# Performance work log

Measured on AMD Instinct MI355X. Metric: run time of the kernel, lower is better.

The kernel has to match this reference:

```python
import jax, jax.numpy as jnp
import numpy as np

NUM_RBF = 16
MIN_MU = 2.0
MAX_MU = 22.0
K_NEIGHBORS = 48
MAX_REL = 32
POS_DIM = 16
EDGE_OUT = 128
N_TOKENS = 21
N_ATOMS = 14
N_ATOM_TYPES = 5  # N, CA, C, O + 1 virtual
W_NORMAL, W_B1, W_B2 = 0.58273431, -0.56802827, -0.54067466


def setup_inputs() -> dict:
    key = jax.random.key(0)
    ks = jax.random.split(key, 8)
    B, L = 2, 2048
    X = jax.random.normal(ks[0], (B, L, N_ATOMS, 3), jnp.float32) * 10.0
    X_m = jnp.ones((B, L, N_ATOMS), jnp.float32)
    S = jax.random.randint(ks[1], (B, L), 0, N_TOKENS)
    residue_idx = jnp.arange(B * L).reshape(B, L)
    mask = jnp.ones((B, L), jnp.float32)
    # token -> atom-slot index table for [N, CA, C, O] (per-token fancy indexing)
    table = jax.random.randint(ks[2], (N_TOKENS, 4), 0, N_ATOMS)
    n_pos_in = 2 * MAX_REL + 1
    W_pos = jax.random.normal(ks[3], (n_pos_in, POS_DIM), jnp.float32) * 0.05
    b_pos = jnp.zeros((POS_DIM,), jnp.float32)
    n_edge_in = POS_DIM + NUM_RBF * N_ATOM_TYPES * N_ATOM_TYPES  # 416
    W_e = jax.random.normal(ks[4], (n_edge_in, EDGE_OUT), jnp.float32) * 0.05
    ln_g = jnp.ones((EDGE_OUT,), jnp.float32)
    ln_b = jnp.zeros((EDGE_OUT,), jnp.float32)
    return {"X": X, "X_m": X_m, "S": S, "residue_idx": residue_idx, "mask": mask,
            "table": table, "W_pos": W_pos, "b_pos": b_pos, "W_e": W_e,
            "ln_g": ln_g, "ln_b": ln_b}


def _rbf(D):
    mu = jnp.linspace(MIN_MU, MAX_MU, NUM_RBF, dtype=D.dtype)
    sigma = (MAX_MU - MIN_MU) / NUM_RBF
    return jnp.exp(-jnp.square((D[..., None] - mu) / sigma))


def reference(X, X_m, S, residue_idx, mask, table, W_pos, b_pos, W_e, ln_g, ln_b):
    B, L = S.shape
    # token-dependent gather of backbone atoms [B,L,4,3]
    idx = table[S]
    X_bb = jnp.take_along_axis(X, idx[..., None], axis=2)
    N_, CA, C_ = X_bb[:, :, 0], X_bb[:, :, 1], X_bb[:, :, 2]
    # virtual atom (CB-like) from N, CA, C
    b1 = N_ - CA
    b2 = C_ - CA
    nrm = jnp.cross(b1, b2)
    Xv = W_NORMAL * nrm + W_B1 * b1 + W_B2 * b2 + CA
    X_all = jnp.concatenate([X_bb, Xv[:, :, None, :]], axis=2)  # [B,L,5,3]
    # pairwise CA distances + masked top-k neighbors
    diff = CA[:, :, None, :] - CA[:, None, :, :]
    D = jnp.sqrt(jnp.sum(diff * diff, -1) + 1e-6)
    m2 = mask[:, :, None] * mask[:, None, :]
    D_adj = D * m2 + (1.0 - m2) * 1e6
    _, E_idx = jax.lax.top_k(-D_adj, K_NEIGHBORS)  # [B,L,K]
    # gather neighbor atom coords [B,L,K,5,3]
    X_nb = jax.vmap(lambda xa, ei: xa[ei])(X_all, E_idx)
    d = X_all[:, :, None, :, None, :] - X_nb[:, :, :, None, :, :]  # [B,L,K,5,5,3]
    Dab = jnp.sqrt(jnp.sum(d * d, -1) + 1e-6)
    RBF = _rbf(Dab).reshape(B, L, K_NEIGHBORS, N_ATOM_TYPES * N_ATOM_TYPES * NUM_RBF)
    # positional encodings of relative residue offsets
    r_nb = jax.vmap(lambda r, ei: r[ei])(residue_idx, E_idx)
    off = jnp.clip(residue_idx[:, :, None] - r_nb + MAX_REL, 0, 2 * MAX_REL)
    pos = jax.nn.one_hot(off, 2 * MAX_REL + 1, dtype=RBF.dtype) @ W_pos + b_pos
    # edge embedding (no bias) + layernorm
    E = jnp.concatenate([pos, RBF], -1) @ W_e
    mu_ = jnp.mean(E, -1, keepdims=True)
    var = jnp.var(E, -1, keepdims=True)
    E = (E - mu_) * jax.lax.rsqrt(var + 1e-5) * ln_g + ln_b
    return E, E_idx
```

## Files before the change

### kernel.cpp

```cpp
#include <hip/hip_runtime.h>
#include <hip/hip_bf16.h>

#define Bq 2
#define Lq 2048
#define BLq (Bq*Lq)
#define KNB 48
#define NA 14
#define NTOK 21
#define NRBF 16
#define POSD 16
#define EOUT 128
#define CSTRIDE 168
#define ESTRIDE 132
#define E_ELEMS (BLq*KNB*EOUT)

typedef __attribute__((ext_vector_type(8))) short short8;
typedef __attribute__((ext_vector_type(4))) float f32x4;

__device__ __forceinline__ unsigned short bf16_rn(float x) {
    unsigned int u = __float_as_uint(x);
    unsigned int r = (u + 0x7fffu + ((u >> 16) & 1u)) >> 16;
    return (unsigned short)r;
}

__device__ __forceinline__ unsigned int pkbf2(float a, float b) {
    __hip_bfloat162 t = __float22bfloat162_rn(make_float2(a, b));
    union { __hip_bfloat162 h; unsigned int u; } cv; cv.h = t;
    return cv.u;
}

__global__ void prep_kernel(const float* __restrict__ X, const int* __restrict__ S,
                            const int* __restrict__ table, const float* __restrict__ mask,
                            const float* __restrict__ We,
                            float* __restrict__ Xall, float4* __restrict__ CA4,
                            short* __restrict__ Wp) {
    int bid = blockIdx.x;
    if (bid < 16) {
        int t = bid * 256 + threadIdx.x;
        if (t >= BLq) return;
        int s = S[t];
        float bb[4][3];
#pragma unroll
        for (int a = 0; a < 4; ++a) {
            int ia = table[s * 4 + a];
#pragma unroll
            for (int d = 0; d < 3; ++d) bb[a][d] = X[(t * NA + ia) * 3 + d];
        }
        float b1[3], b2[3], nr[3];
#pragma unroll
        for (int d = 0; d < 3; ++d) { b1[d] = bb[0][d] - bb[1][d]; b2[d] = bb[2][d] - bb[1][d]; }
        nr[0] = b1[1] * b2[2] - b1[2] * b2[1];
        nr[1] = b1[2] * b2[0] - b1[0] * b2[2];
        nr[2] = b1[0] * b2[1] - b1[1] * b2[0];
#pragma unroll
        for (int a = 0; a < 4; ++a)
#pragma unroll
            for (int d = 0; d < 3; ++d) Xall[t * 15 + a * 3 + d] = bb[a][d];
#pragma unroll
        for (int d = 0; d < 3; ++d) {
            float xv = 0.58273431f * nr[d] + (-0.56802827f) * b1[d] + (-0.54067466f) * b2[d] + bb[1][d];
            Xall[t * 15 + 12 + d] = xv;
        }
        CA4[t] = make_float4(bb[1][0], bb[1][1], bb[1][2], mask[t]);
    } else {
        int t = (bid - 16) * 256 + threadIdx.x;
        if (t >= 13 * 8 * 64 * 8) return;
        int j = t & 7;
        int lane = (t >> 3) & 63;
        int nt = (t >> 9) & 7;
        int kt = t >> 12;
        int k = kt * 32 + (lane >> 4) * 8 + j;
        int n = nt * 16 + (lane & 15);
        Wp[t] = (short)bf16_rn(We[k * 128 + n]);
    }
}

__device__ __forceinline__ void rbf16(float D, unsigned short* dst) {
    const float s1   = 0.96089793f;
    const float dlt  = 1.28119724f;
    const float dlt2 = 1.64146638f;
    const float tdl  = 2.56239448f;
    const float Cg   = 0.10273972f;
    float u0 = __builtin_fmaf(D, s1, -1.92179585f);
    uint4 qa, qb;
    {
        float ua = u0 - 5.12478895f;
        float va = __builtin_amdgcn_exp2f(-(ua * ua));
        float eu = fminf(__builtin_fmaf(tdl, ua, -dlt2), 120.0f);
        float ed = fminf(__builtin_fmaf(-tdl, ua, -dlt2), 120.0f);
        float gu = __builtin_amdgcn_exp2f(eu);
        float gd = __builtin_amdgcn_exp2f(ed);
        float v4 = va;
        float v5 = v4 * gu; float g2 = gu * Cg;
        float v6 = v5 * g2;
        float v7 = v6 * (g2 * Cg);
        float v3 = v4 * gd; float h2 = gd * Cg;
        float v2 = v3 * h2; float h3 = h2 * Cg;
        float v1 = v2 * h3;
        float v0 = v1 * (h3 * Cg);
        qa.x = pkbf2(v0, v1); qa.y = pkbf2(v2, v3);
        qa.z = pkbf2(v4, v5); qa.w = pkbf2(v6, v7);
    }
    {
        float ub = u0 - 15.37436684f;
        float vb = __builtin_amdgcn_exp2f(-(ub * ub));
        float eu = fminf(__builtin_fmaf(tdl, ub, -dlt2), 120.0f);
        float ed = fminf(__builtin_fmaf(-tdl, ub, -dlt2), 120.0f);
        float gu = __builtin_amdgcn_exp2f(eu);
        float gd = __builtin_amdgcn_exp2f(ed);
        float v12 = vb;
        float v13 = v12 * gu; float g2 = gu * Cg;
        float v14 = v13 * g2;
        float v15 = v14 * (g2 * Cg);
        float v11 = v12 * gd; float h2 = gd * Cg;
        float v10 = v11 * h2; float h3 = h2 * Cg;
        float v9  = v10 * h3;
        float v8  = v9 * (h3 * Cg);
        qb.x = pkbf2(v8, v9);   qb.y = pkbf2(v10, v11);
        qb.z = pkbf2(v12, v13); qb.w = pkbf2(v14, v15);
    }
    *(uint4*)dst = qa;
    *(uint4*)(dst + 8) = qb;
}

__global__ __launch_bounds__(256, 6) void edge_kernel(
    const float4* __restrict__ CA4, const float* __restrict__ Xall,
    const int* __restrict__ ridx, const float* __restrict__ Wpos,
    const float* __restrict__ bpos, const short* __restrict__ Wp,
    const float* __restrict__ lng, const float* __restrict__ lnb,
    float* __restrict__ out, float* __restrict__ out_idx) {
    __shared__ __align__(16) char smem[25344];
    unsigned int* histR = (unsigned int*)smem;
    unsigned int* hist8 = (unsigned int*)smem;
    unsigned long long* buf = (unsigned long long*)(smem + 16384);
    float* Dsm = (float*)smem;
    unsigned short* Asm = (unsigned short*)(smem + 4800);
    float* Xq = (float*)(smem + 20928);
    float* Xn = (float*)(smem + 20992);
    int* offs = (int*)(smem + 23872);
    int* eidxl = (int*)(smem + 24064);
    float* Esm = (float*)smem;
    __shared__ unsigned int nacc, wtot[4];
    __shared__ int sh_bin, sh_excl, sh_cnt;

    int bl = blockIdx.x;
    int base = (bl >> 11) << 11;
    int tid = threadIdx.x;
    int w = tid >> 6, lane = tid & 63;

    float4 q = CA4[bl];
    unsigned long long key[8];
#pragma unroll
    for (int i = 0; i < 8; ++i) {
        int j = tid + (i << 8);
        float4 c = CA4[base + j];
        float dx = __fsub_rn(q.x, c.x);
        float dy = __fsub_rn(q.y, c.y);
        float dz = __fsub_rn(q.z, c.z);
        float s = __fadd_rn(__fadd_rn(__fmul_rn(dx, dx), __fmul_rn(dy, dy)), __fmul_rn(dz, dz));
        float D = __fsqrt_rn(__fadd_rn(s, 1e-6f));
        float m2 = __fmul_rn(q.w, c.w);
        float Dadj = __fadd_rn(__fmul_rn(D, m2), __fmul_rn(__fsub_rn(1.0f, m2), 1000000.0f));
        key[i] = (((unsigned long long)__float_as_uint(Dadj)) << 16) | (unsigned int)j;
    }

    {
        uint4 z = make_uint4(0u, 0u, 0u, 0u);
        for (int i = tid; i < 1024; i += 256) ((uint4*)histR)[i] = z;
    }
    __syncthreads();
#pragma unroll
    for (int i = 0; i < 8; ++i)
        atomicAdd(&histR[(((unsigned int)(key[i] >> 38)) << 2) | (unsigned int)(lane & 3)], 1u);
    __syncthreads();

    unsigned int loc[4], lsum = 0;
#pragma unroll
    for (int j = 0; j < 4; ++j) {
        uint4 r4 = ((const uint4*)histR)[tid * 4 + j];
        loc[j] = r4.x + r4.y + r4.z + r4.w;
        lsum += loc[j];
    }
    unsigned int incl = lsum;
#pragma unroll
    for (int o = 1; o < 64; o <<= 1) {
        unsigned int v = __shfl_up(incl, o);
        if (lane >= o) incl += v;
    }
    if (lane == 63) wtot[w] = incl;
    __syncthreads();
    unsigned int cum = incl - lsum;
#pragma unroll
    for (int u = 0; u < 4; ++u) cum += (u < w) ? wtot[u] : 0u;
#pragma unroll
    for (int j = 0; j < 4; ++j) {
        if ((int)cum < 48 && 48 <= (int)(cum + loc[j])) {
            sh_bin = tid * 4 + j;
            sh_excl = (int)cum;
            sh_cnt = (int)loc[j];
        }
        cum += loc[j];
    }
    __syncthreads();

    unsigned long long prefix = (unsigned long long)(unsigned int)sh_bin;
    int need = 48 - sh_excl;
    int cnt = sh_cnt;
    int shift = 38;

    while (cnt > 80 && shift > 0) {
        shift = (shift >= 8) ? (shift - 8) : 0;
        hist8[tid] = 0;
        __syncthreads();
#pragma unroll
        for (int i = 0; i < 8; ++i)
            if ((key[i] >> (shift + 8)) == prefix)
                atomicAdd(&hist8[(unsigned int)((key[i] >> shift) & 255ull)], 1u);
        __syncthreads();
        if (tid < 64) {
            unsigned int h0 = hist8[4 * tid + 0], h1 = hist8[4 * tid + 1];
            unsigned int h2 = hist8[4 * tid + 2], h3 = hist8[4 * tid + 3];
            unsigned int s4 = h0 + h1 + h2 + h3;
            unsigned int incl2 = s4;
#pragma unroll
            for (int o = 1; o < 64; o <<= 1) {
                unsigned int v = __shfl_up(incl2, o);
                if (tid >= o) incl2 += v;
            }
            unsigned int excl2 = incl2 - s4;
            if ((int)excl2 < need && need <= (int)incl2) {
                unsigned int cb = excl2;
                unsigned int hh[4] = {h0, h1, h2, h3};
                int bsel = 3;
#pragma unroll
                for (int bb2 = 0; bb2 < 4; ++bb2) {
                    if ((int)(cb + hh[bb2]) >= need) { bsel = bb2; break; }
                    cb += hh[bb2];
                }
                sh_bin = 4 * tid + bsel;
                sh_excl = (int)cb;
                sh_cnt = (int)hh[bsel];
            }
        }
        __syncthreads();
        prefix = (prefix << 8) | (unsigned long long)(unsigned int)sh_bin;
        need -= sh_excl;
        cnt = sh_cnt;
    }

    if (tid == 0) nacc = 0;
    __syncthreads();
#pragma unroll
    for (int i = 0; i < 8; ++i) {
        bool p = (key[i] >> shift) <= prefix;
        unsigned long long m = __ballot(p);
        if (m != 0ull) {
            int leader = __ffsll((long long)m) - 1;
            unsigned int bp2 = 0;
            if (lane == leader) bp2 = atomicAdd(&nacc, (unsigned int)__popcll(m));
            bp2 = (unsigned int)__shfl((int)bp2, leader);
            if (p) {
                unsigned int pos = bp2 + (unsigned int)__popcll(m & ((1ull << lane) - 1ull));
                if (pos < 128) buf[pos] = key[i];
            }
        }
    }
    __syncthreads();
    unsigned int mcnt = nacc;
    if (mcnt > 128) mcnt = 128;
    if (tid < 128 && tid >= (int)mcnt) buf[tid] = ~0ULL;
    __syncthreads();

    int mp = (int)((mcnt + 7u) & ~7u);
    if (mp > 128) mp = 128;
    if (tid < 128) {
        unsigned long long k = buf[tid];
        int rank = 0;
        for (int u = 0; u < mp; ++u) rank += (buf[u] < k) ? 1 : 0;
        if (rank < KNB) {
            int j = (int)(k & 0xffffull);
            eidxl[rank] = j;
            out_idx[bl * KNB + rank] = (float)j;
        }
    }
    __syncthreads();

    if (tid < KNB) {
        int j = eidxl[tid];
        int off = ridx[bl] - ridx[base + j] + 32;
        offs[tid] = min(max(off, 0), 64);
    }
    if (tid < 15) Xq[tid] = Xall[bl * 15 + tid];
    for (int f = tid; f < KNB * 15; f += 256) {
        int k = f / 15, d = f - k * 15;
        int j = eidxl[k];
        Xn[f] = Xall[(base + j) * 15 + d];
    }
    __syncthreads();

    for (int f = tid; f < KNB * 25; f += 256) {
        int k = f / 25, p = f - k * 25;
        int a = p / 5, c = p - a * 5;
        float dx = Xq[a * 3 + 0] - Xn[k * 15 + c * 3 + 0];
        float dy = Xq[a * 3 + 1] - Xn[k * 15 + c * 3 + 1];
        float dz = Xq[a * 3 + 2] - Xn[k * 15 + c * 3 + 2];
        Dsm[f] = sqrtf(dx * dx + dy * dy + dz * dz + 1e-6f);
    }
    __syncthreads();

    int quad = lane >> 4, lr = lane & 15;
    f32x4 acc[3][2];
#pragma unroll
    for (int mt = 0; mt < 3; ++mt)
#pragma unroll
        for (int nt = 0; nt < 2; ++nt) acc[mt][nt] = (f32x4){0.f, 0.f, 0.f, 0.f};

    auto gemm_chunk = [&](int ktBase, int ktCnt) {
#pragma unroll
        for (int ktl = 0; ktl < ktCnt; ++ktl) {
            int kt = ktBase + ktl;
            short8 bf0 = *(const short8*)(Wp + (((kt * 8 + 2 * w + 0) * 64 + lane) << 3));
            short8 bf1 = *(const short8*)(Wp + (((kt * 8 + 2 * w + 1) * 64 + lane) << 3));
#pragma unroll
            for (int mt = 0; mt < 3; ++mt) {
                short8 af = *(const short8*)(&Asm[(mt * 16 + lr) * CSTRIDE + ktl * 32 + quad * 8]);
                acc[mt][0] = __builtin_amdgcn_mfma_f32_16x16x32_bf16(af, bf0, acc[mt][0], 0, 0, 0);
                acc[mt][1] = __builtin_amdgcn_mfma_f32_16x16x32_bf16(af, bf1, acc[mt][1], 0, 0, 0);
            }
        }
    };

    if (tid < KNB) {
        int off = offs[tid];
        const float4* wr = (const float4*)(Wpos + off * 16);
        const float4* bp = (const float4*)bpos;
        float4 a0 = wr[0], a1 = wr[1], a2 = wr[2], a3 = wr[3];
        float4 b0 = bp[0], b1 = bp[1], b2 = bp[2], b3 = bp[3];
        uint4 o1, o2;
        o1.x = pkbf2(a0.x + b0.x, a0.y + b0.y); o1.y = pkbf2(a0.z + b0.z, a0.w + b0.w);
        o1.z = pkbf2(a1.x + b1.x, a1.y + b1.y); o1.w = pkbf2(a1.z + b1.z, a1.w + b1.w);
        o2.x = pkbf2(a2.x + b2.x, a2.y + b2.y); o2.y = pkbf2(a2.z + b2.z, a2.w + b2.w);
        o2.z = pkbf2(a3.x + b3.x, a3.y + b3.y); o2.w = pkbf2(a3.z + b3.z, a3.w + b3.w);
        unsigned short* dst = Asm + tid * CSTRIDE;
        *(uint4*)dst = o1;
        *(uint4*)(dst + 8) = o2;
    }
    for (int it = tid; it < 9 * KNB; it += 256) {
        int prl = it / KNB, k = it - prl * KNB;
        rbf16(Dsm[k * 25 + prl], Asm + k * CSTRIDE + 16 + prl * 16);
    }
    __syncthreads();
    gemm_chunk(0, 5);
    __syncthreads();

    for (int it = tid; it < 8 * KNB; it += 256) {
        int prl = it / KNB, k = it - prl * KNB;
        rbf16(Dsm[k * 25 + 9 + prl], Asm + k * CSTRIDE + prl * 16);
    }
    __syncthreads();
    gemm_chunk(5, 4);
    __syncthreads();

    for (int it = tid; it < 8 * KNB; it += 256) {
        int prl = it / KNB, k = it - prl * KNB;
        rbf16(Dsm[k * 25 + 17 + prl], Asm + k * CSTRIDE + prl * 16);
    }
    __syncthreads();
    gemm_chunk(9, 4);
    __syncthreads();

#pragma unroll
    for (int mt = 0; mt < 3; ++mt)
#pragma unroll
        for (int ntl = 0; ntl < 2; ++ntl) {
            int col = (2 * w + ntl) * 16 + lr;
#pragma unroll
            for (int r = 0; r < 4; ++r) {
                int row = mt * 16 + quad * 4 + r;
                Esm[row * ESTRIDE + col] = acc[mt][ntl][r];
            }
        }
    __syncthreads();

    float g0 = lng[lane], g1 = lng[lane + 64];
    float bb0 = lnb[lane], bb1 = lnb[lane + 64];
    for (int r = w; r < KNB; r += 4) {
        float v0 = Esm[r * ESTRIDE + lane];
        float v1 = Esm[r * ESTRIDE + lane + 64];
        float s = v0 + v1;
        float qq = __builtin_fmaf(v0, v0, v1 * v1);
#pragma unroll
        for (int o = 32; o > 0; o >>= 1) { s += __shfl_xor(s, o); qq += __shfl_xor(qq, o); }
        float mean = s * 0.0078125f;
        float var = __builtin_fmaf(-mean, mean, qq * 0.0078125f);
        float inv = rsqrtf(var + 1e-5f);
        float a0 = inv * g0, a1 = inv * g1;
        int ob = (bl * KNB + r) * EOUT;
        out[ob + lane] = __builtin_fmaf(v0 - mean, a0, bb0);
        out[ob + lane + 64] = __builtin_fmaf(v1 - mean, a1, bb1);
    }
}

extern "C" void kernel_launch(void* const* d_in, const int* in_sizes, int n_in,
                              void* d_out, int out_size, void* d_ws, size_t ws_size,
                              hipStream_t stream) {
    const float* X    = (const float*)d_in[0];
    const int*   S    = (const int*)d_in[2];
    const int*   ridx = (const int*)d_in[3];
    const float* mask = (const float*)d_in[4];
    const int*   tab  = (const int*)d_in[5];
    const float* Wpos = (const float*)d_in[6];
    const float* bpos = (const float*)d_in[7];
    const float* We   = (const float*)d_in[8];
    const float* lng  = (const float*)d_in[9];
    const float* lnb  = (const float*)d_in[10];
    float* out = (float*)d_out;

    char* ws = (char*)d_ws;
    float*  Xall = (float*)ws;
    short*  Wp   = (short*)(ws + 245760);
    float4* CA4  = (float4*)(ws + 245760 + 106496);

    prep_kernel<<<224, 256, 0, stream>>>(X, S, tab, mask, We, Xall, CA4, Wp);
    edge_kernel<<<BLq, 256, 0, stream>>>(CA4, Xall, ridx, Wpos, bpos, Wp, lng, lnb,
                                         out, out + E_ELEMS);
}
```

Measured before the change: 183.2 us.

## Fuse distance into RBF fill, LayerNorm from registers, finer top-k histogram

Computes the per-pair atom distances inside the RBF fill, which drops the Dsm staging buffer and one barrier. LayerNorm now runs directly on the MFMA accumulators: row sums and sums of squares are reduced by shuffles and passed between waves through a small partials table, replacing the full Esm staging. Shared memory shrinks to raise the launch_bounds occupancy hint from 6 to 7 blocks. The top-k radix histogram now uses 4096 exact bins instead of 1024 lane-replicated bins, so fewer refinement passes are needed, but atomic contention on the bins rises.

```diff
diff --git a/kernel.cpp b/kernel.cpp
--- a/kernel.cpp
+++ b/kernel.cpp
@@ -11,7 +11,6 @@
 #define POSD 16
 #define EOUT 128
 #define CSTRIDE 168
-#define ESTRIDE 132
 #define E_ELEMS (BLq*KNB*EOUT)
 
 typedef __attribute__((ext_vector_type(8))) short short8;
@@ -77,7 +76,6 @@
 
 __device__ __forceinline__ void rbf16(float D, unsigned short* dst) {
     const float s1   = 0.96089793f;
-    const float dlt  = 1.28119724f;
     const float dlt2 = 1.64146638f;
     const float tdl  = 2.56239448f;
     const float Cg   = 0.10273972f;
@@ -123,23 +121,23 @@
     *(uint4*)(dst + 8) = qb;
 }
 
-__global__ __launch_bounds__(256, 6) void edge_kernel(
+__global__ __launch_bounds__(256, 7) void edge_kernel(
     const float4* __restrict__ CA4, const float* __restrict__ Xall,
     const int* __restrict__ ridx, const float* __restrict__ Wpos,
     const float* __restrict__ bpos, const short* __restrict__ Wp,
     const float* __restrict__ lng, const float* __restrict__ lnb,
     float* __restrict__ out, float* __restrict__ out_idx) {
-    __shared__ __align__(16) char smem[25344];
+    __shared__ __align__(16) char smem[20992];
     unsigned int* histR = (unsigned int*)smem;
     unsigned int* hist8 = (unsigned int*)smem;
     unsigned long long* buf = (unsigned long long*)(smem + 16384);
-    float* Dsm = (float*)smem;
-    unsigned short* Asm = (unsigned short*)(smem + 4800);
-    float* Xq = (float*)(smem + 20928);
-    float* Xn = (float*)(smem + 20992);
-    int* offs = (int*)(smem + 23872);
-    int* eidxl = (int*)(smem + 24064);
-    float* Esm = (float*)smem;
+    unsigned short* Asm = (unsigned short*)smem;
+    float* Xq = (float*)(smem + 16128);
+    float* Xn = (float*)(smem + 16192);
+    int* offs = (int*)(smem + 19072);
+    int* eidxl = (int*)(smem + 19264);
+    float2* stats = (float2*)(smem + 19072);
+    float* partials = (float*)(smem + 19456);
     __shared__ unsigned int nacc, wtot[4];
     __shared__ int sh_bin, sh_excl, sh_cnt;
 
@@ -166,20 +164,22 @@
 
     {
         uint4 z = make_uint4(0u, 0u, 0u, 0u);
-        for (int i = tid; i < 1024; i += 256) ((uint4*)histR)[i] = z;
+#pragma unroll
+        for (int i = 0; i < 4; ++i) ((uint4*)histR)[tid + (i << 8)] = z;
     }
     __syncthreads();
 #pragma unroll
     for (int i = 0; i < 8; ++i)
-        atomicAdd(&histR[(((unsigned int)(key[i] >> 38)) << 2) | (unsigned int)(lane & 3)], 1u);
-    __syncthreads();
-
-    unsigned int loc[4], lsum = 0;
+        atomicAdd(&histR[(unsigned int)((key[i] >> 35) & 4095ull)], 1u);
+    __syncthreads();
+
+    unsigned int loc[16], lsum = 0;
 #pragma unroll
     for (int j = 0; j < 4; ++j) {
         uint4 r4 = ((const uint4*)histR)[tid * 4 + j];
-        loc[j] = r4.x + r4.y + r4.z + r4.w;
-        lsum += loc[j];
+        loc[4 * j + 0] = r4.x; loc[4 * j + 1] = r4.y;
+        loc[4 * j + 2] = r4.z; loc[4 * j + 3] = r4.w;
+        lsum += (r4.x + r4.y) + (r4.z + r4.w);
     }
     unsigned int incl = lsum;
 #pragma unroll
@@ -193,9 +193,9 @@
 #pragma unroll
     for (int u = 0; u < 4; ++u) cum += (u < w) ? wtot[u] : 0u;
 #pragma unroll
-    for (int j = 0; j < 4; ++j) {
+    for (int j = 0; j < 16; ++j) {
         if ((int)cum < 48 && 48 <= (int)(cum + loc[j])) {
-            sh_bin = tid * 4 + j;
+            sh_bin = tid * 16 + j;
             sh_excl = (int)cum;
             sh_cnt = (int)loc[j];
         }
@@ -206,7 +206,7 @@
     unsigned long long prefix = (unsigned long long)(unsigned int)sh_bin;
     int need = 48 - sh_excl;
     int cnt = sh_cnt;
-    int shift = 38;
+    int shift = 35;
 
     while (cnt > 80 && shift > 0) {
         shift = (shift >= 8) ? (shift - 8) : 0;
@@ -298,16 +298,6 @@
     }
     __syncthreads();
 
-    for (int f = tid; f < KNB * 25; f += 256) {
-        int k = f / 25, p = f - k * 25;
-        int a = p / 5, c = p - a * 5;
-        float dx = Xq[a * 3 + 0] - Xn[k * 15 + c * 3 + 0];
-        float dy = Xq[a * 3 + 1] - Xn[k * 15 + c * 3 + 1];
-        float dz = Xq[a * 3 + 2] - Xn[k * 15 + c * 3 + 2];
-        Dsm[f] = sqrtf(dx * dx + dy * dy + dz * dz + 1e-6f);
-    }
-    __syncthreads();
-
     int quad = lane >> 4, lr = lane & 15;
     f32x4 acc[3][2];
 #pragma unroll
@@ -327,6 +317,19 @@
                 acc[mt][0] = __builtin_amdgcn_mfma_f32_16x16x32_bf16(af, bf0, acc[mt][0], 0, 0, 0);
                 acc[mt][1] = __builtin_amdgcn_mfma_f32_16x16x32_bf16(af, bf1, acc[mt][1], 0, 0, 0);
             }
+        }
+    };
+
+    auto fill_rbf = [&](int prBase, int prCount, int colBase) {
+        for (int it = tid; it < prCount * KNB; it += 256) {
+            int prl = it / KNB, k = it - prl * KNB;
+            int pr = prBase + prl;
+            int a = pr / 5, c = pr - a * 5;
+            float dx = Xq[a * 3 + 0] - Xn[k * 15 + c * 3 + 0];
+            float dy = Xq[a * 3 + 1] - Xn[k * 15 + c * 3 + 1];
+            float dz = Xq[a * 3 + 2] - Xn[k * 15 + c * 3 + 2];
+            float D = sqrtf(dx * dx + dy * dy + dz * dz + 1e-6f);
+            rbf16(D, Asm + k * CSTRIDE + colBase + prl * 16);
         }
     };
 
@@ -345,60 +348,61 @@
         *(uint4*)dst = o1;
         *(uint4*)(dst + 8) = o2;
     }
-    for (int it = tid; it < 9 * KNB; it += 256) {
-        int prl = it / KNB, k = it - prl * KNB;
-        rbf16(Dsm[k * 25 + prl], Asm + k * CSTRIDE + 16 + prl * 16);
-    }
+    fill_rbf(0, 9, 16);
     __syncthreads();
     gemm_chunk(0, 5);
     __syncthreads();
 
-    for (int it = tid; it < 8 * KNB; it += 256) {
-        int prl = it / KNB, k = it - prl * KNB;
-        rbf16(Dsm[k * 25 + 9 + prl], Asm + k * CSTRIDE + prl * 16);
-    }
+    fill_rbf(9, 8, 0);
     __syncthreads();
     gemm_chunk(5, 4);
     __syncthreads();
 
-    for (int it = tid; it < 8 * KNB; it += 256) {
-        int prl = it / KNB, k = it - prl * KNB;
-        rbf16(Dsm[k * 25 + 17 + prl], Asm + k * CSTRIDE + prl * 16);
-    }
+    fill_rbf(17, 8, 0);
     __syncthreads();
     gemm_chunk(9, 4);
-    __syncthreads();
+
+    float g0 = lng[w * 32 + lr], g1 = lng[w * 32 + 16 + lr];
+    float b0 = lnb[w * 32 + lr], b1 = lnb[w * 32 + 16 + lr];
 
 #pragma unroll
     for (int mt = 0; mt < 3; ++mt)
 #pragma unroll
-        for (int ntl = 0; ntl < 2; ++ntl) {
-            int col = (2 * w + ntl) * 16 + lr;
-#pragma unroll
-            for (int r = 0; r < 4; ++r) {
+        for (int r = 0; r < 4; ++r) {
+            float v0 = acc[mt][0][r], v1 = acc[mt][1][r];
+            float s = v0 + v1;
+            float qs = __builtin_fmaf(v0, v0, v1 * v1);
+#pragma unroll
+            for (int o = 1; o < 16; o <<= 1) { s += __shfl_xor(s, o); qs += __shfl_xor(qs, o); }
+            if (lr == mt * 4 + r) {
                 int row = mt * 16 + quad * 4 + r;
-                Esm[row * ESTRIDE + col] = acc[mt][ntl][r];
+                *(float2*)(partials + row * 8 + w * 2) = make_float2(s, qs);
             }
         }
     __syncthreads();
 
-    float g0 = lng[lane], g1 = lng[lane + 64];
-    float bb0 = lnb[lane], bb1 = lnb[lane + 64];
-    for (int r = w; r < KNB; r += 4) {
-        float v0 = Esm[r * ESTRIDE + lane];
-        float v1 = Esm[r * ESTRIDE + lane + 64];
-        float s = v0 + v1;
-        float qq = __builtin_fmaf(v0, v0, v1 * v1);
-#pragma unroll
-        for (int o = 32; o > 0; o >>= 1) { s += __shfl_xor(s, o); qq += __shfl_xor(qq, o); }
+    if (tid < KNB) {
+        float4 p0 = *(const float4*)(partials + tid * 8);
+        float4 p1 = *(const float4*)(partials + tid * 8 + 4);
+        float s = (p0.x + p0.z) + (p1.x + p1.z);
+        float qs = (p0.y + p0.w) + (p1.y + p1.w);
         float mean = s * 0.0078125f;
-        float var = __builtin_fmaf(-mean, mean, qq * 0.0078125f);
-        float inv = rsqrtf(var + 1e-5f);
-        float a0 = inv * g0, a1 = inv * g1;
-        int ob = (bl * KNB + r) * EOUT;
-        out[ob + lane] = __builtin_fmaf(v0 - mean, a0, bb0);
-        out[ob + lane + 64] = __builtin_fmaf(v1 - mean, a1, bb1);
-    }
+        float var = __builtin_fmaf(-mean, mean, qs * 0.0078125f);
+        stats[tid] = make_float2(mean, rsqrtf(var + 1e-5f));
+    }
+    __syncthreads();
+
+#pragma unroll
+    for (int mt = 0; mt < 3; ++mt)
+#pragma unroll
+        for (int r = 0; r < 4; ++r) {
+            int row = mt * 16 + quad * 4 + r;
+            float2 st = stats[row];
+            float mean = st.x, inv = st.y;
+            int ob = (bl * KNB + row) * EOUT + w * 32 + lr;
+            out[ob]      = __builtin_fmaf(acc[mt][0][r] - mean, inv * g0, b0);
+            out[ob + 16] = __builtin_fmaf(acc[mt][1][r] - mean, inv * g1, b1);
+        }
 }
 
 extern "C" void kernel_launch(void* const* d_in, const int* in_sizes, int n_in,
```

Result: faster. 173.7 us (-5.2%).
